# Kernel optimization log

Hardware: AMD Instinct MI355X
Metric: run time of the kernel (lower is better)

The kernel has to match this reference:

```python
import jax, jax.numpy as jnp
import numpy as np

DELTA_VAR = 0.5
DELTA_DIST = 1.5
ALPHA = 1.0
BETA = 1.0
C = 4096        # number of superpixels (static for segment_sum)
NE = 16384      # number of RAG edges


def setup_inputs() -> dict:
    key = jax.random.key(0)
    k1, k2, k3, k4 = jax.random.split(key, 4)
    embeddings = jax.random.normal(k1, (1, 16, 1024, 1024), dtype=jnp.float32)
    sp_seg = jax.random.randint(k2, (1, 1, 1024, 1024), 0, C)
    edges = jax.random.randint(k3, (2, NE), 0, C)
    weights = jax.random.uniform(k4, (NE,), dtype=jnp.float32)
    return {"embeddings": embeddings, "weights": weights, "sp_seg": sp_seg, "edges": edges}


def reference(embeddings, weights, sp_seg, edges):
    # embeddings: (1,E,H,W); sp_seg: (1,1,H,W) int labels in [0,C)
    E = embeddings.shape[1]
    emb = embeddings.reshape(E, -1).T          # (P,E) pixel-major
    seg = sp_seg.reshape(-1)                   # (P,)
    counts = jax.ops.segment_sum(jnp.ones(seg.shape, emb.dtype), seg, num_segments=C)  # (C,)
    sums = jax.ops.segment_sum(emb, seg, num_segments=C)                               # (C,E)
    n = jnp.maximum(counts, 1.0)               # guard empty segments (orig would div-by-0)
    means = sums / n[:, None]                  # (C,E) superpixel mean embeddings
    # intra-superpixel: d = 1 - <mean_c, emb_p> at pixels of segment c, hinge at delta_var,
    # normalized per-pixel by segment size, then averaged over C
    d_intra = 1.0 - jnp.sum(means[seg] * emb, axis=-1)            # (P,)
    intra = jnp.sum(jnp.maximum(d_intra - DELTA_VAR, 0.0) / n[seg]) / C
    # inter-superpixel: gather edge endpoint means, weighted hinge at delta_dist
    u, v = edges[0], edges[1]
    d_inter = 1.0 - jnp.sum(means[u] * means[v], axis=-1)         # (Ne,)
    inter = jnp.sum(jnp.maximum(DELTA_DIST - d_inter * weights, 0.0)) / edges.shape[1]
    return ALPHA * inter + BETA * intra
```

## Files before the change

### kernel.cpp

```cpp
#include <hip/hip_runtime.h>

#define C_SEG 4096
#define E_CH 16
#define NE_EDGES 16384
#define P_PIX (1024 * 1024)
#define NCHUNK 32
#define CHUNK_PIX (P_PIX / NCHUNK)
#define SCALE 262144.0f
#define INV_SCALE (1.0f / 262144.0f)
#define BIAS 4194304


__global__ __launch_bounds__(512) void kA(const float* __restrict__ emb,
                                          const int* __restrict__ seg,
                                          int* __restrict__ sums_raw,
                                          int* __restrict__ cnt_raw) {
    __shared__ unsigned long long bins[C_SEG];
    const int chunk = blockIdx.x;
    const int g = blockIdx.y;
    const int t = threadIdx.x;
    const int base = chunk * CHUNK_PIX;

    if (g == 8) {
        int* ib = (int*)bins;
        for (int i = t; i < C_SEG; i += 512) ib[i] = 0;
        __syncthreads();
        for (int it = 0; it < 16; ++it) {
            const int idx = base + (it * 512 + t) * 4;
            const int4 s4 = *(const int4*)(seg + idx);
            atomicAdd(&ib[s4.x], 1);
            atomicAdd(&ib[s4.y], 1);
            atomicAdd(&ib[s4.z], 1);
            atomicAdd(&ib[s4.w], 1);
        }
        __syncthreads();
        int* cd = cnt_raw + (size_t)chunk * C_SEG;
        for (int i = t; i < C_SEG; i += 512) cd[i] = ib[i];
    } else {
        for (int i = t; i < C_SEG; i += 512) bins[i] = 0ull;
        __syncthreads();
        const float* ea = emb + (size_t)(2 * g) * P_PIX;
        const float* eb = emb + (size_t)(2 * g + 1) * P_PIX;
        for (int it = 0; it < 16; ++it) {
            const int idx = base + (it * 512 + t) * 4;
            const int4 s4 = *(const int4*)(seg + idx);
            const float4 va = *(const float4*)(ea + idx);
            const float4 vb = *(const float4*)(eb + idx);
            const unsigned long long p0 =
                ((unsigned long long)(unsigned)(__float2int_rn(vb.x * SCALE) + BIAS) << 32) |
                (unsigned)(__float2int_rn(va.x * SCALE) + BIAS);
            const unsigned long long p1 =
                ((unsigned long long)(unsigned)(__float2int_rn(vb.y * SCALE) + BIAS) << 32) |
                (unsigned)(__float2int_rn(va.y * SCALE) + BIAS);
            const unsigned long long p2 =
                ((unsigned long long)(unsigned)(__float2int_rn(vb.z * SCALE) + BIAS) << 32) |
                (unsigned)(__float2int_rn(va.z * SCALE) + BIAS);
            const unsigned long long p3 =
                ((unsigned long long)(unsigned)(__float2int_rn(vb.w * SCALE) + BIAS) << 32) |
                (unsigned)(__float2int_rn(va.w * SCALE) + BIAS);
            atomicAdd(&bins[s4.x], p0);
            atomicAdd(&bins[s4.y], p1);
            atomicAdd(&bins[s4.z], p2);
            atomicAdd(&bins[s4.w], p3);
        }
        __syncthreads();
        int* da = sums_raw + ((size_t)(2 * g) * NCHUNK + chunk) * C_SEG;
        int* db = sums_raw + ((size_t)(2 * g + 1) * NCHUNK + chunk) * C_SEG;
        for (int i = t; i < C_SEG; i += 512) {
            const unsigned long long v = bins[i];
            da[i] = (int)(unsigned)(v & 0xffffffffull);
            db[i] = (int)(unsigned)(v >> 32);
        }
    }
}

__global__ __launch_bounds__(256) void kB(const int* __restrict__ sums_raw,
                                          const int* __restrict__ cnt_raw,
                                          float* __restrict__ mean,
                                          float* __restrict__ inv_n) {
    const int vb = blockIdx.x, t = threadIdx.x;
    const int c = vb >> 4;
    const int s = (vb & 15) * 256 + t;
    const int* src = sums_raw + (size_t)c * NCHUNK * C_SEG + s;
    long long acc = 0;
    int cnt = 0;
#pragma unroll
    for (int k = 0; k < NCHUNK; ++k) {
        acc += src[(size_t)k * C_SEG];
        cnt += cnt_raw[(size_t)k * C_SEG + s];
    }
    acc -= (long long)cnt * (long long)BIAS;
    const float invn = 1.0f / fmaxf((float)cnt, 1.0f);
    mean[s * E_CH + c] = (float)acc * INV_SCALE * invn;
    if (c == 0) inv_n[s] = invn;
}

__global__ __launch_bounds__(256) void kC(const float* __restrict__ emb,
                                          const int* __restrict__ seg,
                                          const int* __restrict__ edges,
                                          const float* __restrict__ w,
                                          const float* __restrict__ mean,
                                          const float* __restrict__ inv_n,
                                          float* __restrict__ part) {
    const int b = blockIdx.x, t = threadIdx.x;
    const int q = b * 256 + t;
    const int2 s2 = *(const int2*)(seg + q * 2);

    float mA[16], mB[16];
#pragma unroll
    for (int j = 0; j < 4; ++j) {
        ((float4*)mA)[j] = ((const float4*)(mean + s2.x * E_CH))[j];
        ((float4*)mB)[j] = ((const float4*)(mean + s2.y * E_CH))[j];
    }
    const float inx = inv_n[s2.x], iny = inv_n[s2.y];

    const float2* emb2 = (const float2*)emb;
    float2 e[16];
#pragma unroll
    for (int c = 0; c < 16; ++c) e[c] = emb2[(size_t)c * (P_PIX / 2) + q];

    float dx = 0.f, dy = 0.f;
#pragma unroll
    for (int c = 0; c < 16; ++c) {
        dx = fmaf(e[c].x, mA[c], dx);
        dy = fmaf(e[c].y, mB[c], dy);
    }

    float v = (fmaxf(0.5f - dx, 0.0f) * inx +
               fmaxf(0.5f - dy, 0.0f) * iny) *
              (1.0f / (float)C_SEG);

    if (t < 8) {
        const int e2 = b * 8 + t;
        const int u = edges[e2];
        const int vv = edges[NE_EDGES + e2];
        const float4* mu = (const float4*)(mean + u * E_CH);
        const float4* mv = (const float4*)(mean + vv * E_CH);
        float dot = 0.0f;
#pragma unroll
        for (int j = 0; j < 4; ++j) {
            const float4 a = mu[j];
            const float4 bb = mv[j];
            dot = fmaf(a.x, bb.x, dot);
            dot = fmaf(a.y, bb.y, dot);
            dot = fmaf(a.z, bb.z, dot);
            dot = fmaf(a.w, bb.w, dot);
        }
        const float d = 1.0f - dot;
        v += fmaxf(1.5f - d * w[e2], 0.0f) * (1.0f / (float)NE_EDGES);
    }

    for (int o = 32; o > 0; o >>= 1) v += __shfl_down(v, o, 64);
    __shared__ float red[4];
    if ((t & 63) == 0) red[t >> 6] = v;
    __syncthreads();
    if (t == 0) part[b] = red[0] + red[1] + red[2] + red[3];
}

__global__ __launch_bounds__(256) void kF(const float* __restrict__ part,
                                          float* __restrict__ out) {
    float v = 0.0f;
    for (int i = threadIdx.x; i < 2048; i += 256) v += part[i];
    for (int o = 32; o > 0; o >>= 1) v += __shfl_down(v, o, 64);
    __shared__ float red[4];
    const int t = threadIdx.x;
    if ((t & 63) == 0) red[t >> 6] = v;
    __syncthreads();
    if (t == 0) out[0] = red[0] + red[1] + red[2] + red[3];
}

extern "C" void kernel_launch(void* const* d_in, const int* in_sizes, int n_in,
                              void* d_out, int out_size, void* d_ws,
                              size_t ws_size, hipStream_t stream) {
    const float* emb = (const float*)d_in[0];
    const float* weights = (const float*)d_in[1];
    const int* seg = (const int*)d_in[2];
    const int* edges = (const int*)d_in[3];
    float* out = (float*)d_out;

    char* ws = (char*)d_ws;
    int* sums_raw = (int*)(ws);
    int* cnt_raw = (int*)(ws + 0x800000);
    float* mean = (float*)(ws + 0x880000);
    float* invn = (float*)(ws + 0x8C0000);
    float* part = (float*)(ws + 0x8C4000);

    dim3 gA(NCHUNK, 9);
    kA<<<gA, 512, 0, stream>>>(emb, seg, sums_raw, cnt_raw);
    kB<<<256, 256, 0, stream>>>(sums_raw, cnt_raw, mean, invn);
    kC<<<2048, 256, 0, stream>>>(emb, seg, edges, weights, mean, invn, part);
    kF<<<1, 256, 0, stream>>>(part, out);
}
```

Before: 142.4 us.

## Split histogram to one channel per block with 32-bit LDS atomics, double chunks

The segment-sum kernel now gives each block a single embedding channel and does 32-bit shared-memory atomics, replacing the packed 64-bit two-channel atomics. The count is folded into the upper half of channel 0's 64-bit bin, which removes the separate count-only block row. The chunk count is doubled, so the grid grows from 288 to 1024 blocks with half the pixels each. The aim is more parallelism and cheaper atomics, at the cost of reading seg 16 times instead of 9 and writing twice as many partial histograms for kB to reduce.

```diff
diff --git a/kernel.cpp b/kernel.cpp
--- a/kernel.cpp
+++ b/kernel.cpp
@@ -4,7 +4,7 @@
 #define E_CH 16
 #define NE_EDGES 16384
 #define P_PIX (1024 * 1024)
-#define NCHUNK 32
+#define NCHUNK 64
 #define CHUNK_PIX (P_PIX / NCHUNK)
 #define SCALE 262144.0f
 #define INV_SCALE (1.0f / 262144.0f)
@@ -15,62 +15,50 @@
                                           const int* __restrict__ seg,
                                           int* __restrict__ sums_raw,
                                           int* __restrict__ cnt_raw) {
-    __shared__ unsigned long long bins[C_SEG];
+    __shared__ unsigned long long bins64[C_SEG];
+    int* ib = (int*)bins64;
     const int chunk = blockIdx.x;
     const int g = blockIdx.y;
     const int t = threadIdx.x;
     const int base = chunk * CHUNK_PIX;
+    const float* ec = emb + (size_t)g * P_PIX;
 
-    if (g == 8) {
-        int* ib = (int*)bins;
+    if (g == 0) {
+        for (int i = t; i < C_SEG; i += 512) bins64[i] = 0ull;
+        __syncthreads();
+        for (int it = 0; it < 8; ++it) {
+            const int idx = base + (it * 512 + t) * 4;
+            const int4 s4 = *(const int4*)(seg + idx);
+            const float4 v = *(const float4*)(ec + idx);
+            const unsigned long long ONE_HI = 1ull << 32;
+            atomicAdd(&bins64[s4.x], ONE_HI | (unsigned)(__float2int_rn(v.x * SCALE) + BIAS));
+            atomicAdd(&bins64[s4.y], ONE_HI | (unsigned)(__float2int_rn(v.y * SCALE) + BIAS));
+            atomicAdd(&bins64[s4.z], ONE_HI | (unsigned)(__float2int_rn(v.z * SCALE) + BIAS));
+            atomicAdd(&bins64[s4.w], ONE_HI | (unsigned)(__float2int_rn(v.w * SCALE) + BIAS));
+        }
+        __syncthreads();
+        int* da = sums_raw + (size_t)chunk * C_SEG;
+        int* cd = cnt_raw + (size_t)chunk * C_SEG;
+        for (int i = t; i < C_SEG; i += 512) {
+            const unsigned long long v = bins64[i];
+            da[i] = (int)(unsigned)(v & 0xffffffffull);
+            cd[i] = (int)(unsigned)(v >> 32);
+        }
+    } else {
         for (int i = t; i < C_SEG; i += 512) ib[i] = 0;
         __syncthreads();
-        for (int it = 0; it < 16; ++it) {
+        for (int it = 0; it < 8; ++it) {
             const int idx = base + (it * 512 + t) * 4;
             const int4 s4 = *(const int4*)(seg + idx);
-            atomicAdd(&ib[s4.x], 1);
-            atomicAdd(&ib[s4.y], 1);
-            atomicAdd(&ib[s4.z], 1);
-            atomicAdd(&ib[s4.w], 1);
+            const float4 v = *(const float4*)(ec + idx);
+            atomicAdd(&ib[s4.x], __float2int_rn(v.x * SCALE) + BIAS);
+            atomicAdd(&ib[s4.y], __float2int_rn(v.y * SCALE) + BIAS);
+            atomicAdd(&ib[s4.z], __float2int_rn(v.z * SCALE) + BIAS);
+            atomicAdd(&ib[s4.w], __float2int_rn(v.w * SCALE) + BIAS);
         }
         __syncthreads();
-        int* cd = cnt_raw + (size_t)chunk * C_SEG;
-        for (int i = t; i < C_SEG; i += 512) cd[i] = ib[i];
-    } else {
-        for (int i = t; i < C_SEG; i += 512) bins[i] = 0ull;
-        __syncthreads();
-        const float* ea = emb + (size_t)(2 * g) * P_PIX;
-        const float* eb = emb + (size_t)(2 * g + 1) * P_PIX;
-        for (int it = 0; it < 16; ++it) {
-            const int idx = base + (it * 512 + t) * 4;
-            const int4 s4 = *(const int4*)(seg + idx);
-            const float4 va = *(const float4*)(ea + idx);
-            const float4 vb = *(const float4*)(eb + idx);
-            const unsigned long long p0 =
-                ((unsigned long long)(unsigned)(__float2int_rn(vb.x * SCALE) + BIAS) << 32) |
-                (unsigned)(__float2int_rn(va.x * SCALE) + BIAS);
-            const unsigned long long p1 =
-                ((unsigned long long)(unsigned)(__float2int_rn(vb.y * SCALE) + BIAS) << 32) |
-                (unsigned)(__float2int_rn(va.y * SCALE) + BIAS);
-            const unsigned long long p2 =
-                ((unsigned long long)(unsigned)(__float2int_rn(vb.z * SCALE) + BIAS) << 32) |
-                (unsigned)(__float2int_rn(va.z * SCALE) + BIAS);
-            const unsigned long long p3 =
-                ((unsigned long long)(unsigned)(__float2int_rn(vb.w * SCALE) + BIAS) << 32) |
-                (unsigned)(__float2int_rn(va.w * SCALE) + BIAS);
-            atomicAdd(&bins[s4.x], p0);
-            atomicAdd(&bins[s4.y], p1);
-            atomicAdd(&bins[s4.z], p2);
-            atomicAdd(&bins[s4.w], p3);
-        }
-        __syncthreads();
-        int* da = sums_raw + ((size_t)(2 * g) * NCHUNK + chunk) * C_SEG;
-        int* db = sums_raw + ((size_t)(2 * g + 1) * NCHUNK + chunk) * C_SEG;
-        for (int i = t; i < C_SEG; i += 512) {
-            const unsigned long long v = bins[i];
-            da[i] = (int)(unsigned)(v & 0xffffffffull);
-            db[i] = (int)(unsigned)(v >> 32);
-        }
+        int* dst = sums_raw + ((size_t)g * NCHUNK + chunk) * C_SEG;
+        for (int i = t; i < C_SEG; i += 512) dst[i] = ib[i];
     }
 }
 
@@ -180,12 +168,12 @@
 
     char* ws = (char*)d_ws;
     int* sums_raw = (int*)(ws);
-    int* cnt_raw = (int*)(ws + 0x800000);
-    float* mean = (float*)(ws + 0x880000);
-    float* invn = (float*)(ws + 0x8C0000);
-    float* part = (float*)(ws + 0x8C4000);
+    int* cnt_raw = (int*)(ws + 0x1000000);
+    float* mean = (float*)(ws + 0x1100000);
+    float* invn = (float*)(ws + 0x1140000);
+    float* part = (float*)(ws + 0x1144000);
 
-    dim3 gA(NCHUNK, 9);
+    dim3 gA(NCHUNK, 16);
     kA<<<gA, 512, 0, stream>>>(emb, seg, sums_raw, cnt_raw);
     kB<<<256, 256, 0, stream>>>(sums_raw, cnt_raw, mean, invn);
     kC<<<2048, 256, 0, stream>>>(emb, seg, edges, weights, mean, invn, part);
```

Result: slower. 155.2 us (+8.9%).
